# Kernel tuning notes

Hardware: AMD Instinct MI355X
Metric: run time of the kernel (lower is better)

Reference implementation:

```python
import jax, jax.numpy as jnp
import numpy as np

E = 1_000_000
D_IN = 64
D_OUT = 64
N_TYPES = 8


def setup_inputs() -> dict:
    key = jax.random.key(0)
    k1, k2, k3, k4 = jax.random.split(key, 4)
    edge_features = jax.random.normal(k1, (E, D_IN), dtype=jnp.float32)
    edge_types = jax.random.randint(k2, (E,), 0, N_TYPES, dtype=jnp.int64)
    # per-type Linear params: W[t] is [in, out], b[t] is [out]
    W = jax.random.normal(k3, (N_TYPES, D_IN, D_OUT), dtype=jnp.float32) * (1.0 / np.sqrt(D_IN))
    b = jax.random.normal(k4, (N_TYPES, D_OUT), dtype=jnp.float32) * 0.01
    return {"edge_features": edge_features, "edge_types": edge_types, "W": W, "b": b}


def reference(edge_features, edge_types, W, b):
    # Per-edge-type Linear + ReLU, scattered back by type mask.
    # Loop is over the small fixed set of edge types (structurally distinct
    # weight matrices), not over the edge data dimension.
    out = jnp.zeros((edge_features.shape[0], D_OUT), dtype=edge_features.dtype)
    for t in range(N_TYPES):
        y = jax.nn.relu(edge_features @ W[t] + b[t])  # [E, D_OUT]
        mask = (edge_types == t)[:, None]
        out = jnp.where(mask, y, out)
    return out
```

## Files before the change

### kernel.cpp

```cpp
#include <hip/hip_runtime.h>
#include <stdint.h>

#define D 64
#define NT 8
#define BLOCK 256
#define TPB 16

typedef __attribute__((ext_vector_type(8))) short short8;
typedef __attribute__((ext_vector_type(4))) float f32x4;

__device__ __forceinline__ unsigned pkbf(float lo, float hi) {
    unsigned r;
    asm("v_cvt_pk_bf16_f32 %0, %1, %2" : "=v"(r) : "v"(lo), "v"(hi));
    return r;
}

__global__ void __launch_bounds__(BLOCK, 2)
edge_mlp_kernel(const float* __restrict__ ef, const int* __restrict__ types,
                const float* __restrict__ W, const float* __restrict__ Bv,
                float* __restrict__ out, int E)
{
    __shared__ unsigned WT[NT * 2048];
    __shared__ float BIAS[NT * D];

    const int tid = threadIdx.x;

    {
        const int t  = tid >> 5;
        const int k0 = (tid & 31) * 2;
        const float* w0 = W + (size_t)t * (D * D) + (size_t)k0 * D;
#pragma unroll
        for (int c4 = 0; c4 < D; c4 += 4) {
            f32x4 ra = *(const f32x4*)(w0 + c4);
            f32x4 rb = *(const f32x4*)(w0 + D + c4);
#pragma unroll
            for (int j = 0; j < 4; ++j) {
                const int c = c4 + j;
                unsigned idx = (unsigned)(t * 2048 + c * 32 + (k0 >> 1));
                idx ^= (unsigned)((c & 7) << 2);
                WT[idx] = pkbf(ra[j], rb[j]);
            }
        }
        BIAS[tid]       = Bv[tid];
        BIAS[tid + 256] = Bv[tid + 256];
    }
    __syncthreads();

    const int wave = tid >> 6;
    const int lane = tid & 63;
    const int n = lane & 15;
    const int g = lane >> 4;
    const int ntiles = (E + 63) >> 6;

    for (int it = 0; it < 4; ++it) {
        const int ti = blockIdx.x * TPB + wave * 4 + it;
        if (ti >= ntiles) break;
        const int tb = ti << 6;

        int eidx = tb + lane; if (eidx >= E) eidx = E - 1;
        const int t_lane = types[eidx];

        f32x4 a[4][4];
#pragma unroll
        for (int mt = 0; mt < 4; ++mt) {
            int row = tb + mt * 16 + n; if (row >= E) row = E - 1;
            const float* rp = ef + (size_t)row * D + g * 8;
            a[mt][0] = *(const f32x4*)(rp);
            a[mt][1] = *(const f32x4*)(rp + 4);
            a[mt][2] = *(const f32x4*)(rp + 32);
            a[mt][3] = *(const f32x4*)(rp + 36);
        }

        short8 fa[4][2];
#pragma unroll
        for (int mt = 0; mt < 4; ++mt) {
            union { unsigned u[4]; short8 s; } u0, u1;
            u0.u[0] = pkbf(a[mt][0][0], a[mt][0][1]);
            u0.u[1] = pkbf(a[mt][0][2], a[mt][0][3]);
            u0.u[2] = pkbf(a[mt][1][0], a[mt][1][1]);
            u0.u[3] = pkbf(a[mt][1][2], a[mt][1][3]);
            u1.u[0] = pkbf(a[mt][2][0], a[mt][2][1]);
            u1.u[1] = pkbf(a[mt][2][2], a[mt][2][3]);
            u1.u[2] = pkbf(a[mt][3][0], a[mt][3][1]);
            u1.u[3] = pkbf(a[mt][3][2], a[mt][3][3]);
            fa[mt][0] = u0.s;
            fa[mt][1] = u1.s;
        }

        int tt[4];
#pragma unroll
        for (int mt = 0; mt < 4; ++mt) tt[mt] = __shfl(t_lane, mt * 16 + n);

        f32x4 acc[4][4];
#pragma unroll
        for (int mt = 0; mt < 4; ++mt)
#pragma unroll
            for (int nb = 0; nb < 4; ++nb) acc[mt][nb] = (f32x4){0.f, 0.f, 0.f, 0.f};

        for (int t = 0; t < NT; ++t) {
            short8 bf[2][4];
#pragma unroll
            for (int kb = 0; kb < 2; ++kb)
#pragma unroll
                for (int nb = 0; nb < 4; ++nb) {
                    const int col = nb * 16 + n;
                    unsigned idx = (unsigned)(t * 2048 + col * 32 + kb * 16 + g * 4);
                    idx ^= (unsigned)((col & 7) << 2);
                    bf[kb][nb] = *(const short8*)&WT[idx];
                }
            const short8 z = (short8)0;
#pragma unroll
            for (int mt = 0; mt < 4; ++mt) {
                const bool m = (tt[mt] == t);
                short8 ma0 = m ? fa[mt][0] : z;
                short8 ma1 = m ? fa[mt][1] : z;
#pragma unroll
                for (int nb = 0; nb < 4; ++nb) {
                    acc[mt][nb] = __builtin_amdgcn_mfma_f32_16x16x32_bf16(ma0, bf[0][nb], acc[mt][nb], 0, 0, 0);
                    acc[mt][nb] = __builtin_amdgcn_mfma_f32_16x16x32_bf16(ma1, bf[1][nb], acc[mt][nb], 0, 0, 0);
                }
            }
        }

#pragma unroll
        for (int mt = 0; mt < 4; ++mt) {
#pragma unroll
            for (int r = 0; r < 4; ++r) {
                const int lrow = mt * 16 + g * 4 + r;
                const int row  = tb + lrow;
                const int trow = __shfl(t_lane, lrow);
                if (row < E) {
                    float* orow = out + (size_t)row * D;
#pragma unroll
                    for (int nb = 0; nb < 4; ++nb) {
                        float v = acc[mt][nb][r] + BIAS[trow * D + nb * 16 + n];
                        orow[nb * 16 + n] = v > 0.f ? v : 0.f;
                    }
                }
            }
        }
    }
}

extern "C" void kernel_launch(void* const* d_in, const int* in_sizes, int n_in,
                              void* d_out, int out_size, void* d_ws, size_t ws_size,
                              hipStream_t stream) {
    const float* ef    = (const float*)d_in[0];
    const int*   types = (const int*)d_in[1];
    const float* W     = (const float*)d_in[2];
    const float* Bv    = (const float*)d_in[3];
    float* out = (float*)d_out;
    const int E = in_sizes[1];
    const int ntiles = (E + 63) / 64;
    const int grid = (ntiles + TPB - 1) / TPB;
    hipLaunchKernelGGL(edge_mlp_kernel, dim3(grid), dim3(BLOCK), 0, stream,
                       ef, types, W, Bv, out, E);
}
```

Measured before the change: 447.3 us.

## Prefetch next tile's features in registers, pad bias LDS, use nontemporal stores

Software-pipelines the per-wave tile loop so the global loads of the next 64-edge tile's features and types are issued before the current tile's MFMA work, hiding memory latency. Pads the bias shared-memory rows from 64 to 68 floats to spread LDS bank accesses, and writes outputs with nontemporal stores to avoid cache pollution. The prefetch doubles the live feature registers, which may increase register pressure against the two-blocks-per-CU launch bound, and adds one redundant final prefetch per wave.

```diff
diff --git a/kernel.cpp b/kernel.cpp
--- a/kernel.cpp
+++ b/kernel.cpp
@@ -5,6 +5,7 @@
 #define NT 8
 #define BLOCK 256
 #define TPB 16
+#define ITERS 4
 
 typedef __attribute__((ext_vector_type(8))) short short8;
 typedef __attribute__((ext_vector_type(4))) float f32x4;
@@ -21,7 +22,7 @@
                 float* __restrict__ out, int E)
 {
     __shared__ unsigned WT[NT * 2048];
-    __shared__ float BIAS[NT * D];
+    __shared__ float BIAS[NT * 68];
 
     const int tid = threadIdx.x;
 
@@ -41,8 +42,11 @@
                 WT[idx] = pkbf(ra[j], rb[j]);
             }
         }
-        BIAS[tid]       = Bv[tid];
-        BIAS[tid + 256] = Bv[tid + 256];
+#pragma unroll
+        for (int q = 0; q < 2; ++q) {
+            const int idx = tid + q * 256;
+            BIAS[(idx >> 6) * 68 + (idx & 63)] = Bv[idx];
+        }
     }
     __syncthreads();
 
@@ -51,45 +55,66 @@
     const int n = lane & 15;
     const int g = lane >> 4;
     const int ntiles = (E + 63) >> 6;
+    const int tlast = ntiles - 1;
 
-    for (int it = 0; it < 4; ++it) {
-        const int ti = blockIdx.x * TPB + wave * 4 + it;
-        if (ti >= ntiles) break;
-        const int tb = ti << 6;
+    const int ti0 = blockIdx.x * TPB + wave * ITERS;
 
-        int eidx = tb + lane; if (eidx >= E) eidx = E - 1;
-        const int t_lane = types[eidx];
-
-        f32x4 a[4][4];
+    f32x4 an[4][4];
+    int tln;
+    {
+        const int pb = min(ti0, tlast) << 6;
+        tln = types[min(pb + lane, E - 1)];
 #pragma unroll
         for (int mt = 0; mt < 4; ++mt) {
-            int row = tb + mt * 16 + n; if (row >= E) row = E - 1;
+            const int row = min(pb + mt * 16 + n, E - 1);
             const float* rp = ef + (size_t)row * D + g * 8;
-            a[mt][0] = *(const f32x4*)(rp);
-            a[mt][1] = *(const f32x4*)(rp + 4);
-            a[mt][2] = *(const f32x4*)(rp + 32);
-            a[mt][3] = *(const f32x4*)(rp + 36);
+            an[mt][0] = *(const f32x4*)(rp);
+            an[mt][1] = *(const f32x4*)(rp + 4);
+            an[mt][2] = *(const f32x4*)(rp + 32);
+            an[mt][3] = *(const f32x4*)(rp + 36);
         }
+    }
+
+#pragma unroll
+    for (int it = 0; it < ITERS; ++it) {
+        const int tcur = ti0 + it;
+        if (tcur >= ntiles) break;
+        const int tb = tcur << 6;
 
         short8 fa[4][2];
 #pragma unroll
         for (int mt = 0; mt < 4; ++mt) {
             union { unsigned u[4]; short8 s; } u0, u1;
-            u0.u[0] = pkbf(a[mt][0][0], a[mt][0][1]);
-            u0.u[1] = pkbf(a[mt][0][2], a[mt][0][3]);
-            u0.u[2] = pkbf(a[mt][1][0], a[mt][1][1]);
-            u0.u[3] = pkbf(a[mt][1][2], a[mt][1][3]);
-            u1.u[0] = pkbf(a[mt][2][0], a[mt][2][1]);
-            u1.u[1] = pkbf(a[mt][2][2], a[mt][2][3]);
-            u1.u[2] = pkbf(a[mt][3][0], a[mt][3][1]);
-            u1.u[3] = pkbf(a[mt][3][2], a[mt][3][3]);
+            u0.u[0] = pkbf(an[mt][0][0], an[mt][0][1]);
+            u0.u[1] = pkbf(an[mt][0][2], an[mt][0][3]);
+            u0.u[2] = pkbf(an[mt][1][0], an[mt][1][1]);
+            u0.u[3] = pkbf(an[mt][1][2], an[mt][1][3]);
+            u1.u[0] = pkbf(an[mt][2][0], an[mt][2][1]);
+            u1.u[1] = pkbf(an[mt][2][2], an[mt][2][3]);
+            u1.u[2] = pkbf(an[mt][3][0], an[mt][3][1]);
+            u1.u[3] = pkbf(an[mt][3][2], an[mt][3][3]);
             fa[mt][0] = u0.s;
             fa[mt][1] = u1.s;
+        }
+        const int tl = tln;
+
+        {
+            const int pb = min(tcur + 1, tlast) << 6;
+            tln = types[min(pb + lane, E - 1)];
+#pragma unroll
+            for (int mt = 0; mt < 4; ++mt) {
+                const int row = min(pb + mt * 16 + n, E - 1);
+                const float* rp = ef + (size_t)row * D + g * 8;
+                an[mt][0] = *(const f32x4*)(rp);
+                an[mt][1] = *(const f32x4*)(rp + 4);
+                an[mt][2] = *(const f32x4*)(rp + 32);
+                an[mt][3] = *(const f32x4*)(rp + 36);
+            }
         }
 
         int tt[4];
 #pragma unroll
-        for (int mt = 0; mt < 4; ++mt) tt[mt] = __shfl(t_lane, mt * 16 + n);
+        for (int mt = 0; mt < 4; ++mt) tt[mt] = __shfl(tl, mt * 16 + n);
 
         f32x4 acc[4][4];
 #pragma unroll
@@ -128,13 +153,14 @@
             for (int r = 0; r < 4; ++r) {
                 const int lrow = mt * 16 + g * 4 + r;
                 const int row  = tb + lrow;
-                const int trow = __shfl(t_lane, lrow);
+                const int trow = __shfl(tl, lrow);
                 if (row < E) {
                     float* orow = out + (size_t)row * D;
 #pragma unroll
                     for (int nb = 0; nb < 4; ++nb) {
-                        float v = acc[mt][nb][r] + BIAS[trow * D + nb * 16 + n];
-                        orow[nb * 16 + n] = v > 0.f ? v : 0.f;
+                        float v = acc[mt][nb][r] + BIAS[trow * 68 + nb * 16 + n];
+                        v = v > 0.f ? v : 0.f;
+                        __builtin_nontemporal_store(v, &orow[nb * 16 + n]);
                     }
                 }
             }
```

After: 471.9 us. 5.5% more time.
